# Optimization experiments

Measured on AMD Instinct MI355X. Metric: run time of the kernel, lower is better.

Reference implementation:

```python
import jax, jax.numpy as jnp
import numpy as np

NHEAD, DK, DV = 8, 32, 32
GRAPH = [[1,2,3,6,7],[1,2,4],[1,3,5],[2,4],[3,5],[1,6,8,12],[1,7,9,13],[6,8,10],[7,9,13],[8,10],[9,11],[9,12,14],[11,13,15],[12,14,16],[13,15,17],[14,16],[15,17]]
_idx = np.zeros((17,5), np.int32); _val = np.zeros((17,5), bool)
for _i, _nb in enumerate(GRAPH):
    for _j, _n in enumerate(_nb):
        _idx[_i,_j] = _n-1; _val[_i,_j] = True
NBR_IDX = jnp.asarray(_idx)            # (17,5) neighbor table (pad idx 0)
NBR_VALID = jnp.asarray(_val)          # (17,5) valid-neighbor mask
ATT_MASK = jnp.asarray(np.concatenate([_val, np.ones((17,2), bool)], 1))  # (17,7): 5 local + 2 global keys
INV_SQRT_DK = float(1.0/np.sqrt(DK))

def _ln_c(x, g, b, eps=1e-6):
    # LayerNorm over channel axis of (B,C,L)
    m = x.mean(1, keepdims=True)
    v = x.var(1, keepdims=True)
    return (x - m) * jax.lax.rsqrt(v + eps) * g[None,:,None] + b[None,:,None]

def _bn3(x, g, b, eps=1e-5):
    # BatchNorm1d (training batch stats) per channel over (B,L); x:(B,C,L)
    m = x.mean((0,2), keepdims=True)
    v = x.var((0,2), keepdims=True)
    return (x - m) * jax.lax.rsqrt(v + eps) * g[None,:,None] + b[None,:,None]

def _pos_ffn(x, w1, b1, w2, b2, g, b):
    # x:(B,C,L); Linear over C, relu, Linear back, residual, BatchNorm1d
    h = jax.nn.relu(jnp.einsum('bcl,hc->bhl', x, w1) + b1[None,:,None])
    y = jnp.einsum('bhl,ch->bcl', h, w2) + b2[None,:,None] + x
    return _bn3(y, g, b)

def _unfold(t):
    # t:(B,C,17) -> (B,C,5,17): per-node 5-wide neighbor window, zero padded
    g = t[:,:,NBR_IDX]                              # (B,C,17,5)
    g = jnp.where(NBR_VALID[None,None], g, 0.0)
    return jnp.transpose(g, (0,1,3,2))

def _sju(xn, ax, wq,bq,wk,bk,wv,bv, bng,bnb, f1w,f1b,f2w,f2b,fg,fb):
    B, C, L = xn.shape
    q = (jnp.einsum('oc,bcl->bol', wq, xn) + bq[None,:,None]).reshape(B,NHEAD,DK,L)
    kx = jnp.einsum('oc,bcl->bol', wk, xn) + bk[None,:,None]
    vx = jnp.einsum('oc,bcl->bol', wv, xn) + bv[None,:,None]
    k = _unfold(kx).reshape(B,NHEAD,DK,5,L)
    v = _unfold(vx).reshape(B,NHEAD,DV,5,L)
    ak = (jnp.einsum('oc,bcal->boal', wk, ax) + bk[None,:,None,None]).reshape(B,NHEAD,DK,2,L)
    av = (jnp.einsum('oc,bcal->boal', wv, ax) + bv[None,:,None,None]).reshape(B,NHEAD,DV,2,L)
    k = jnp.concatenate([k, ak], 3)                 # (B,H,dk,7,L)
    v = jnp.concatenate([v, av], 3)
    pre = jnp.einsum('bhdl,bhdwl->bhwl', q, k) * INV_SQRT_DK
    pre = jnp.where(ATT_MASK.T[None,None], pre, -jnp.inf)
    a = jax.nn.softmax(pre, axis=2)
    att = jnp.einsum('bhwl,bhdwl->bhdl', a, v).reshape(B,C,L)
    ret = _bn3(xn + att, bng, bnb)
    return _pos_ffn(ret, f1w,f1b,f2w,f2b,fg,fb)

def _sru(x, y, wq,bq,wk,bk,wv,bv, bng,bnb, f1w,f1b,f2w,f2b,fg,fb):
    # x:(B,C) relay, y:(B,C,Ly) keys/values
    B, C = x.shape
    q = (x @ wq.T + bq).reshape(B,NHEAD,DK)
    k = (jnp.einsum('oc,bcl->bol', wk, y) + bk[None,:,None]).reshape(B,NHEAD,DK,-1)
    v = (jnp.einsum('oc,bcl->bol', wv, y) + bv[None,:,None]).reshape(B,NHEAD,DV,-1)
    a = jax.nn.softmax(jnp.einsum('bhd,bhdl->bhl', q, k) * INV_SQRT_DK, axis=2)
    att = jnp.einsum('bhl,bhdl->bhd', a, v).reshape(B,C)
    ret = _bn3((x + att)[:,:,None], bng, bnb)
    return _pos_ffn(ret, f1w,f1b,f2w,f2b,fg,fb)[:,:,0]

def _forward(data, ln_g, ln_b, jq_w, jq_b, jk_w, jk_b, jv_w, jv_b, jbn_g, jbn_b, jf1_w, jf1_b, jf2_w, jf2_b, jfbn_g, jfbn_b, rq_w, rq_b, rk_w, rk_b, rv_w, rv_b, rbn_g, rbn_b, rf1_w, rf1_b, rf2_w, rf2_b, rfbn_g, rfbn_b):
    B, C, V, T = data.shape
    embs = jnp.transpose(data, (0,3,1,2)).reshape(B*T, C, V)   # fold time into batch
    nodes = embs
    relay = embs.mean(2)                                       # (BT,C)
    # ax: per node the 2 extra keys = its own original embedding + relay (fixed across layers)
    ax = jnp.stack([embs, jnp.broadcast_to(relay[:,:,None], embs.shape)], axis=2)  # (BT,C,2,V)
    for i in range(ln_g.shape[0]):
        xn = _ln_c(nodes, ln_g[i], ln_b[i])
        nodes = jax.nn.leaky_relu(_sju(xn, ax, jq_w[i],jq_b[i],jk_w[i],jk_b[i],jv_w[i],jv_b[i],jbn_g[i],jbn_b[i],jf1_w[i],jf1_b[i],jf2_w[i],jf2_b[i],jfbn_g[i],jfbn_b[i]), 0.01)
        y = jnp.concatenate([relay[:,:,None], nodes], axis=2)   # (BT,C,18)
        relay = jax.nn.leaky_relu(_sru(relay, y, rq_w[i],rq_b[i],rk_w[i],rk_b[i],rv_w[i],rv_b[i],rbn_g[i],rbn_b[i],rf1_w[i],rf1_b[i],rf2_w[i],rf2_b[i],rfbn_g[i],rfbn_b[i]), 0.01)
    return jnp.transpose(nodes.reshape(B,T,C,V), (0,2,3,1))

def setup_inputs():
    key = jax.random.key(0)
    Lyr, C, DIN, B, T, V = 2, 256, 1024, 4, 256, 17
    ks = jax.random.split(key, 40)
    ctr = [0]
    def nxt():
        k = ks[ctr[0]]; ctr[0] += 1; return k
    def w(shape, s=0.05):
        return jax.random.normal(nxt(), shape, jnp.float32) * s
    ones = lambda: jnp.ones((Lyr, C), jnp.float32)
    zeros = lambda: jnp.zeros((Lyr, C), jnp.float32)
    inp = {'data': jax.random.normal(nxt(), (B,C,V,T), jnp.float32),
           'ln_g': ones(), 'ln_b': zeros()}
    for p in ('j', 'r'):
        inp[p+'q_w'] = w((Lyr,C,C)); inp[p+'q_b'] = w((Lyr,C))
        inp[p+'k_w'] = w((Lyr,C,C)); inp[p+'k_b'] = w((Lyr,C))
        inp[p+'v_w'] = w((Lyr,C,C)); inp[p+'v_b'] = w((Lyr,C))
        inp[p+'bn_g'] = ones(); inp[p+'bn_b'] = zeros()
        inp[p+'f1_w'] = w((Lyr,DIN,C)); inp[p+'f1_b'] = w((Lyr,DIN))
        inp[p+'f2_w'] = w((Lyr,C,DIN)); inp[p+'f2_b'] = w((Lyr,C))
        inp[p+'fbn_g'] = ones(); inp[p+'fbn_b'] = zeros()
    return inp

def reference(data, ln_g, ln_b, jq_w, jq_b, jk_w, jk_b, jv_w, jv_b, jbn_g, jbn_b, jf1_w, jf1_b, jf2_w, jf2_b, jfbn_g, jfbn_b, rq_w, rq_b, rk_w, rk_b, rv_w, rv_b, rbn_g, rbn_b, rf1_w, rf1_b, rf2_w, rf2_b, rfbn_g, rfbn_b):
    return _forward(data, ln_g, ln_b, jq_w, jq_b, jk_w, jk_b, jv_w, jv_b, jbn_g, jbn_b, jf1_w, jf1_b, jf2_w, jf2_b, jfbn_g, jfbn_b, rq_w, rq_b, rk_w, rk_b, rv_w, rv_b, rbn_g, rbn_b, rf1_w, rf1_b, rf2_w, rf2_b, rfbn_g, rfbn_b)
```

## Files before the change

kernel.cpp:

```cpp
#include <hip/hip_runtime.h>
#include <hip/hip_bf16.h>


using bf16 = __hip_bfloat16;
typedef __attribute__((ext_vector_type(8))) short bf16x8v;
typedef __attribute__((ext_vector_type(4))) float f32x4;

namespace {
constexpr int kBT = 1024;
constexpr int kC = 256;
constexpr int kV = 17;
constexpr int kT = 256;
constexpr int kDIN = 1024;
constexpr int kRows = kBT * kV;
constexpr int kRowsE = kRows + kBT;
constexpr float kInvSqrtDk = 0.17677669529663687f;
constexpr size_t SZ_BIG = (size_t)kRows * kC;
}

__constant__ int c_nbi[17][5] = {
    {0, 1, 2, 5, 6},   {0, 1, 3, 0, 0},   {0, 2, 4, 0, 0},  {1, 3, 0, 0, 0},
    {2, 4, 0, 0, 0},   {0, 5, 7, 11, 0},  {0, 6, 8, 12, 0}, {5, 7, 9, 0, 0},
    {6, 8, 12, 0, 0},  {7, 9, 0, 0, 0},   {8, 10, 0, 0, 0}, {8, 11, 13, 0, 0},
    {10, 12, 14, 0, 0},{11, 13, 15, 0, 0},{12, 14, 16, 0, 0},
    {13, 15, 0, 0, 0}, {14, 16, 0, 0, 0}};
__constant__ int c_ncnt[17] = {5, 3, 3, 2, 2, 4, 4, 3, 3, 2, 2, 3, 3, 3, 3, 2, 2};

__device__ inline float bf2f(unsigned short s) {
  unsigned int u = ((unsigned int)s) << 16;
  float f;
  __builtin_memcpy(&f, &u, 4);
  return f;
}
__device__ inline unsigned short f2bf(float f) {
  unsigned int u;
  __builtin_memcpy(&u, &f, 4);
  unsigned int r = (u + 0x7fffu + ((u >> 16) & 1u)) >> 16;
  return (unsigned short)r;
}
__device__ inline float4 ldbf4(const bf16* p) {
  ushort4 u = *(const ushort4*)p;
  return make_float4(bf2f(u.x), bf2f(u.y), bf2f(u.z), bf2f(u.w));
}
__device__ inline void stbf4(bf16* p, float4 v) {
  ushort4 u = make_ushort4(f2bf(v.x), f2bf(v.y), f2bf(v.z), f2bf(v.w));
  *(ushort4*)p = u;
}
__device__ inline float dot4(float4 a, float4 b) {
  return a.x * b.x + a.y * b.y + a.z * b.z + a.w * b.w;
}

__device__ inline void async16(const bf16* g, bf16* l) {
  __builtin_amdgcn_global_load_lds(
      (const __attribute__((address_space(1))) void*)g,
      (__attribute__((address_space(3))) void*)l, 16, 0, 0);
}

template <int KT>
__global__ __launch_bounds__(256) void k_mfma_gemm(
    const bf16* __restrict__ A, const bf16* __restrict__ W,
    const float* __restrict__ bias, const float* __restrict__ res,
    float* __restrict__ outF, bf16* __restrict__ outB,
    const float* __restrict__ bnScI, const float* __restrict__ bnShI,
    float* __restrict__ partOut, int nbPart, int N, int flags) {
  __shared__ bf16 As[2][128 * 64];
  __shared__ bf16 Bs[2][128 * 64];
  const int tid = threadIdx.x;
  const int wave = tid >> 6;
  const int lane = tid & 63;
  const int row0 = blockIdx.x * 128;
  const int col0 = blockIdx.y * 128;

  const int sub = lane >> 2;
  const int kq = (lane & 3) * 8;
  const int rg0 = (2 * wave + 0) * 16;
  const int rg1 = (2 * wave + 1) * 16;
  const bf16* ag0 = A + (size_t)(row0 + rg0 + sub) * KT + kq;
  const bf16* ag1 = A + (size_t)(row0 + rg1 + sub) * KT + kq;
  const bf16* bg0 = W + (size_t)(col0 + rg0 + sub) * KT + kq;
  const bf16* bg1 = W + (size_t)(col0 + rg1 + sub) * KT + kq;

  const int wm = wave >> 1, wn = wave & 1;
  const int fr = lane & 15;
  const int fk = (lane >> 4) * 8;

  f32x4 acc[4][4];
#pragma unroll
  for (int i = 0; i < 4; ++i)
#pragma unroll
    for (int j = 0; j < 4; ++j) acc[i][j] = (f32x4){0.f, 0.f, 0.f, 0.f};

#define STAGE64(buf, koff)                                   \
  do {                                                       \
    _Pragma("unroll") for (int kc = 0; kc < 2; ++kc) {       \
      const int off = (koff) + kc * 32;                      \
      async16(ag0 + off, &As[(buf)][kc * 4096 + rg0 * 32]);  \
      async16(ag1 + off, &As[(buf)][kc * 4096 + rg1 * 32]);  \
      async16(bg0 + off, &Bs[(buf)][kc * 4096 + rg0 * 32]);  \
      async16(bg1 + off, &Bs[(buf)][kc * 4096 + rg1 * 32]);  \
    }                                                        \
  } while (0)

  STAGE64(0, 0);
  __syncthreads();

  for (int k0 = 0; k0 < KT; k0 += 64) {
    const int cur = (k0 >> 6) & 1;
    if (k0 + 64 < KT) STAGE64(cur ^ 1, k0 + 64);
#pragma unroll
    for (int kc = 0; kc < 2; ++kc) {
      bf16x8v af[4], bfv[4];
#pragma unroll
      for (int i = 0; i < 4; ++i)
        af[i] = *(const bf16x8v*)&As[cur][kc * 4096 +
                                          (wm * 64 + i * 16 + fr) * 32 + fk];
#pragma unroll
      for (int j = 0; j < 4; ++j)
        bfv[j] = *(const bf16x8v*)&Bs[cur][kc * 4096 +
                                           (wn * 64 + j * 16 + fr) * 32 + fk];
#pragma unroll
      for (int i = 0; i < 4; ++i)
#pragma unroll
        for (int j = 0; j < 4; ++j)
          acc[i][j] = __builtin_amdgcn_mfma_f32_16x16x32_bf16(af[i], bfv[j],
                                                              acc[i][j], 0, 0,
                                                              0);
    }
    __syncthreads();
  }
#undef STAGE64

  if (flags & 4) {
    unsigned short* cs = (unsigned short*)As;
#pragma unroll
    for (int j = 0; j < 4; ++j) {
      int lc = wn * 64 + j * 16 + fr;
      float bv = bias ? bias[col0 + lc] : 0.f;
#pragma unroll
      for (int i = 0; i < 4; ++i) {
        int lr = wm * 64 + i * 16 + (lane >> 4) * 4;
#pragma unroll
        for (int r = 0; r < 4; ++r) {
          float v = acc[i][j][r] + bv;
          if (flags & 1) v = fmaxf(v, 0.f);
          cs[(lr + r) * 128 + lc] = f2bf(v);
        }
      }
    }
    __syncthreads();
#pragma unroll
    for (int p = 0; p < 8; ++p) {
      int lr = p * 16 + (tid >> 4);
      int lc = (tid & 15) * 8;
      *(bf16x8v*)&outB[(size_t)(row0 + lr) * N + col0 + lc] =
          *(const bf16x8v*)&cs[lr * 128 + lc];
    }
  } else {
    const int crow = row0 + wm * 64;
    const int ccol = col0 + wn * 64;
    float colS[4] = {0.f, 0.f, 0.f, 0.f};
    float colQ[4] = {0.f, 0.f, 0.f, 0.f};
#pragma unroll
    for (int j = 0; j < 4; ++j) {
      int col = ccol + j * 16 + fr;
      float bv = bias ? bias[col] : 0.f;
      float rsc = 1.f, rsh = 0.f;
      if (flags & 8) { rsc = bnScI[col]; rsh = bnShI[col]; }
#pragma unroll
      for (int i = 0; i < 4; ++i) {
        int rowb = crow + i * 16 + (lane >> 4) * 4;
#pragma unroll
        for (int r = 0; r < 4; ++r) {
          size_t row = (size_t)(rowb + r);
          float v = acc[i][j][r] + bv;
          if (res) v += res[row * N + col] * rsc + rsh;
          if (flags & 1) v = fmaxf(v, 0.f);
          outF[row * N + col] = v;
          colS[j] += v;
          colQ[j] += v * v;
        }
      }
    }
    if (flags & 8) {
#pragma unroll
      for (int j = 0; j < 4; ++j) {
        colS[j] += __shfl_xor(colS[j], 16);
        colS[j] += __shfl_xor(colS[j], 32);
        colQ[j] += __shfl_xor(colQ[j], 16);
        colQ[j] += __shfl_xor(colQ[j], 32);
      }
      float* sred = (float*)As;
      float* qred = sred + 4 * 64;
      if (lane < 16) {
#pragma unroll
        for (int j = 0; j < 4; ++j) {
          sred[wave * 64 + j * 16 + fr] = colS[j];
          qred[wave * 64 + j * 16 + fr] = colQ[j];
        }
      }
      __syncthreads();
      if (tid < 128) {
        int wn2 = tid >> 6, c = tid & 63;
        float s = sred[wn2 * 64 + c] + sred[(wn2 | 2) * 64 + c];
        float q = qred[wn2 * 64 + c] + qred[(wn2 | 2) * 64 + c];
        int col = col0 + wn2 * 64 + c;
        partOut[(size_t)blockIdx.x * kC + col] = s;
        partOut[(size_t)(nbPart + blockIdx.x) * kC + col] = q;
      }
    }
  }
}

__global__ __launch_bounds__(256) void k_xform_in(const float* __restrict__ data,
                                                  float* __restrict__ nodes,
                                                  bf16* __restrict__ embs_bf) {
  __shared__ float tile[32][33];
  int ct = blockIdx.x * 32, tt = blockIdx.y * 32;
  int bv = blockIdx.z;
  int b = bv / kV, v = bv - b * kV;
  int tx = threadIdx.x & 31, ty = threadIdx.x >> 5;
  for (int i = ty; i < 32; i += 8)
    tile[i][tx] = data[(((size_t)b * kC + ct + i) * kV + v) * kT + tt + tx];
  __syncthreads();
  for (int i = ty; i < 32; i += 8) {
    size_t s = (size_t)b * kT + tt + i;
    size_t idx = (s * kV + v) * kC + ct + tx;
    float val = tile[tx][i];
    nodes[idx] = val;
    embs_bf[idx] = __float2bfloat16(val);
  }
}

__global__ __launch_bounds__(256) void k_xform_out(const float* __restrict__ Z,
                                                   const float* __restrict__ scale,
                                                   const float* __restrict__ shift,
                                                   float* __restrict__ out) {
  __shared__ float tile[32][33];
  int ct = blockIdx.x * 32, tt = blockIdx.y * 32;
  int bv = blockIdx.z;
  int b = bv / kV, v = bv - b * kV;
  int tx = threadIdx.x & 31, ty = threadIdx.x >> 5;
  float sc = scale[ct + tx], sh = shift[ct + tx];
  for (int i = ty; i < 32; i += 8) {
    size_t s = (size_t)b * kT + tt + i;
    float val = Z[(s * kV + v) * kC + ct + tx] * sc + sh;
    val = (val > 0.f) ? val : 0.01f * val;
    tile[i][tx] = val;
  }
  __syncthreads();
  for (int i = ty; i < 32; i += 8)
    out[(((size_t)b * kC + ct + i) * kV + v) * kT + tt + tx] = tile[tx][i];
}

__global__ __launch_bounds__(256) void k_relay_init(const float* __restrict__ nodes,
                                                    bf16* __restrict__ relay0_bf) {
  int t = threadIdx.x;
  int s = blockIdx.x * 4 + (t >> 6);
  int c4 = (t & 63) * 4;
  float4 acc = make_float4(0.f, 0.f, 0.f, 0.f);
#pragma unroll
  for (int v = 0; v < kV; ++v) {
    float4 x = *(const float4*)(nodes + ((size_t)s * kV + v) * kC + c4);
    acc.x += x.x; acc.y += x.y; acc.z += x.z; acc.w += x.w;
  }
  float4 r = make_float4(acc.x / 17.f, acc.y / 17.f, acc.z / 17.f, acc.w / 17.f);
  stbf4(relay0_bf + (size_t)s * kC + c4, r);
}

__global__ __launch_bounds__(256) void k_layernorm(const float* __restrict__ X,
                                                   const float* __restrict__ g,
                                                   const float* __restrict__ b,
                                                   float* __restrict__ O,
                                                   bf16* __restrict__ Ob) {
  int t = threadIdx.x;
  int row = blockIdx.x * 4 + (t >> 6);
  int c4 = (t & 63) * 4;
  size_t i = (size_t)row * kC + c4;
  float4 x = *(const float4*)(X + i);
  float s = x.x + x.y + x.z + x.w;
  float q = dot4(x, x);
#pragma unroll
  for (int o = 32; o >= 1; o >>= 1) {
    s += __shfl_xor(s, o);
    q += __shfl_xor(q, o);
  }
  float m = s * (1.f / 256.f);
  float var = q * (1.f / 256.f) - m * m;
  float rs = rsqrtf(var + 1e-6f);
  float4 g4 = *(const float4*)(g + c4);
  float4 b4 = *(const float4*)(b + c4);
  float4 o4 = make_float4((x.x - m) * rs * g4.x + b4.x,
                          (x.y - m) * rs * g4.y + b4.y,
                          (x.z - m) * rs * g4.z + b4.z,
                          (x.w - m) * rs * g4.w + b4.w);
  *(float4*)(O + i) = o4;
  stbf4(Ob + i, o4);
}

__global__ __launch_bounds__(256) void k_attn_sat(const bf16* __restrict__ qkv,
                                                  const bf16* __restrict__ akav,
                                                  float* __restrict__ z,
                                                  float* __restrict__ part,
                                                  int nb) {
  __shared__ float sS[4][256];
  __shared__ float qS[4][256];
  int t = threadIdx.x;
  int w = t >> 6;
  int rl = blockIdx.x * 4 + w;
  int lane = t & 63;
  int s = rl / kV, l = rl - s * kV;
  int c4 = lane * 4;
  float4 q = ldbf4(qkv + (size_t)rl * 768 + c4);
  int cnt = c_ncnt[l];
  float sc[7];
  int nrow[5];
#pragma unroll
  for (int wd = 0; wd < 5; ++wd) {
    nrow[wd] = s * kV + c_nbi[l][wd];
    float4 k = ldbf4(qkv + (size_t)nrow[wd] * 768 + 256 + c4);
    float p = dot4(q, k);
    p += __shfl_xor(p, 1, 8);
    p += __shfl_xor(p, 2, 8);
    p += __shfl_xor(p, 4, 8);
    sc[wd] = (wd < cnt) ? p * kInvSqrtDk : -1e30f;
  }
  {
    float4 k = ldbf4(akav + (size_t)rl * 1024 + c4);
    float p = dot4(q, k);
    p += __shfl_xor(p, 1, 8);
    p += __shfl_xor(p, 2, 8);
    p += __shfl_xor(p, 4, 8);
    sc[5] = p * kInvSqrtDk;
  }
  {
    float4 k = ldbf4(akav + (size_t)(kRows + s) * 1024 + c4);
    float p = dot4(q, k);
    p += __shfl_xor(p, 1, 8);
    p += __shfl_xor(p, 2, 8);
    p += __shfl_xor(p, 4, 8);
    sc[6] = p * kInvSqrtDk;
  }
  float mx = sc[0];
#pragma unroll
  for (int wd = 1; wd < 7; ++wd) mx = fmaxf(mx, sc[wd]);
  float den = 0.f;
#pragma unroll
  for (int wd = 0; wd < 7; ++wd) {
    sc[wd] = __expf(sc[wd] - mx);
    den += sc[wd];
  }
  float inv = 1.f / den;
  float4 acc = make_float4(0.f, 0.f, 0.f, 0.f);
#pragma unroll
  for (int wd = 0; wd < 5; ++wd) {
    float4 v = ldbf4(qkv + (size_t)nrow[wd] * 768 + 512 + c4);
    acc.x += sc[wd] * v.x; acc.y += sc[wd] * v.y;
    acc.z += sc[wd] * v.z; acc.w += sc[wd] * v.w;
  }
  {
    float4 v = ldbf4(akav + (size_t)rl * 1024 + 256 + c4);
    acc.x += sc[5] * v.x; acc.y += sc[5] * v.y;
    acc.z += sc[5] * v.z; acc.w += sc[5] * v.w;
  }
  {
    float4 v = ldbf4(akav + (size_t)(kRows + s) * 1024 + 256 + c4);
    acc.x += sc[6] * v.x; acc.y += sc[6] * v.y;
    acc.z += sc[6] * v.z; acc.w += sc[6] * v.w;
  }
  size_t zi = (size_t)rl * kC + c4;
  float4 xv = *(const float4*)(z + zi);
  float4 o = make_float4(xv.x + acc.x * inv, xv.y + acc.y * inv,
                         xv.z + acc.z * inv, xv.w + acc.w * inv);
  *(float4*)(z + zi) = o;
  sS[w][c4 + 0] = o.x; sS[w][c4 + 1] = o.y;
  sS[w][c4 + 2] = o.z; sS[w][c4 + 3] = o.w;
  qS[w][c4 + 0] = o.x * o.x; qS[w][c4 + 1] = o.y * o.y;
  qS[w][c4 + 2] = o.z * o.z; qS[w][c4 + 3] = o.w * o.w;
  __syncthreads();
  float ps = sS[0][t] + sS[1][t] + sS[2][t] + sS[3][t];
  float pq = qS[0][t] + qS[1][t] + qS[2][t] + qS[3][t];
  part[(size_t)blockIdx.x * kC + t] = ps;
  part[(size_t)(nb + blockIdx.x) * kC + t] = pq;
}

__global__ __launch_bounds__(256) void k_bn_finalize(const float* __restrict__ part,
                                                     int nb, float inv_n,
                                                     const float* __restrict__ g,
                                                     const float* __restrict__ b,
                                                     float* __restrict__ scale,
                                                     float* __restrict__ shift) {
  int c = blockIdx.x;
  int t = threadIdx.x;
  float s = 0.f, q = 0.f;
  for (int i = t; i < nb; i += 256) {
    s += part[(size_t)i * kC + c];
    q += part[(size_t)(nb + i) * kC + c];
  }
#pragma unroll
  for (int o = 32; o >= 1; o >>= 1) {
    s += __shfl_xor(s, o);
    q += __shfl_xor(q, o);
  }
  __shared__ float ws[4], wq[4];
  int wid = t >> 6;
  if ((t & 63) == 0) { ws[wid] = s; wq[wid] = q; }
  __syncthreads();
  if (t == 0) {
    float S = ws[0] + ws[1] + ws[2] + ws[3];
    float Q = wq[0] + wq[1] + wq[2] + wq[3];
    float m = S * inv_n;
    float var = Q * inv_n - m * m;
    float sc = g[c] * rsqrtf(var + 1e-5f);
    scale[c] = sc;
    shift[c] = b[c] - m * sc;
  }
}

__global__ __launch_bounds__(256) void k_bn_apply(const float* __restrict__ Z,
                                                  const float* __restrict__ scale,
                                                  const float* __restrict__ shift,
                                                  float* __restrict__ outF,
                                                  bf16* __restrict__ outB,
                                                  int leaky) {
  int t = threadIdx.x;
  int row = blockIdx.x * 4 + (t >> 6);
  int c4 = (t & 63) * 4;
  size_t i = (size_t)row * kC + c4;
  float4 z = *(const float4*)(Z + i);
  float4 sc = *(const float4*)(scale + c4);
  float4 sh = *(const float4*)(shift + c4);
  float4 v = make_float4(z.x * sc.x + sh.x, z.y * sc.y + sh.y,
                         z.z * sc.z + sh.z, z.w * sc.w + sh.w);
  if (leaky) {
    v.x = (v.x > 0.f) ? v.x : 0.01f * v.x;
    v.y = (v.y > 0.f) ? v.y : 0.01f * v.y;
    v.z = (v.z > 0.f) ? v.z : 0.01f * v.z;
    v.w = (v.w > 0.f) ? v.w : 0.01f * v.w;
  }
  if (outF) *(float4*)(outF + i) = v;
  if (outB) stbf4(outB + i, v);
}

__global__ __launch_bounds__(256) void k_bn_ln(
    const float* __restrict__ Z, const float* __restrict__ scale,
    const float* __restrict__ shift, const float* __restrict__ g,
    const float* __restrict__ b, float* __restrict__ xnOut,
    bf16* __restrict__ actOut) {
  int t = threadIdx.x;
  int row = blockIdx.x * 4 + (t >> 6);
  int c4 = (t & 63) * 4;
  size_t i = (size_t)row * kC + c4;
  float4 z = *(const float4*)(Z + i);
  float4 sc = *(const float4*)(scale + c4);
  float4 sh = *(const float4*)(shift + c4);
  float4 v = make_float4(z.x * sc.x + sh.x, z.y * sc.y + sh.y,
                         z.z * sc.z + sh.z, z.w * sc.w + sh.w);
  v.x = (v.x > 0.f) ? v.x : 0.01f * v.x;
  v.y = (v.y > 0.f) ? v.y : 0.01f * v.y;
  v.z = (v.z > 0.f) ? v.z : 0.01f * v.z;
  v.w = (v.w > 0.f) ? v.w : 0.01f * v.w;
  float s = v.x + v.y + v.z + v.w;
  float q = dot4(v, v);
#pragma unroll
  for (int o = 32; o >= 1; o >>= 1) {
    s += __shfl_xor(s, o);
    q += __shfl_xor(q, o);
  }
  float m = s * (1.f / 256.f);
  float var = q * (1.f / 256.f) - m * m;
  float rs = rsqrtf(var + 1e-6f);
  float4 g4 = *(const float4*)(g + c4);
  float4 b4 = *(const float4*)(b + c4);
  float4 o4 = make_float4((v.x - m) * rs * g4.x + b4.x,
                          (v.y - m) * rs * g4.y + b4.y,
                          (v.z - m) * rs * g4.z + b4.z,
                          (v.w - m) * rs * g4.w + b4.w);
  *(float4*)(xnOut + i) = o4;
  stbf4(actOut + i, o4);
}

struct CvtTab {
  const float* src[12];
  bf16* dst[12];
  int n[12];
};
__global__ __launch_bounds__(256) void k_cvt_multi(CvtTab t) {
  int c = blockIdx.y;
  int i = (blockIdx.x * 256 + threadIdx.x) * 4;
  if (i >= t.n[c]) return;
  float4 v = *(const float4*)(t.src[c] + i);
  stbf4(t.dst[c] + i, v);
}

struct BiasTab {
  const float* src[10];
  float* dst[10];
};
__global__ __launch_bounds__(256) void k_bias_cat(BiasTab t) {
  t.dst[blockIdx.x][threadIdx.x] = t.src[blockIdx.x][threadIdx.x];
}

extern "C" void kernel_launch(void* const* d_in, const int* in_sizes, int n_in,
                              void* d_out, int out_size, void* d_ws, size_t ws_size,
                              hipStream_t stream) {
  const float* data = (const float*)d_in[0];
  const float* ln_g = (const float*)d_in[1];
  const float* ln_b = (const float*)d_in[2];
  const float* jq_w = (const float*)d_in[3];
  const float* jq_b = (const float*)d_in[4];
  const float* jk_w = (const float*)d_in[5];
  const float* jk_b = (const float*)d_in[6];
  const float* jv_w = (const float*)d_in[7];
  const float* jv_b = (const float*)d_in[8];
  const float* jbn_g = (const float*)d_in[9];
  const float* jbn_b = (const float*)d_in[10];
  const float* jf1_w = (const float*)d_in[11];
  const float* jf1_b = (const float*)d_in[12];
  const float* jf2_w = (const float*)d_in[13];
  const float* jf2_b = (const float*)d_in[14];
  const float* jfbn_g = (const float*)d_in[15];
  const float* jfbn_b = (const float*)d_in[16];
  float* out = (float*)d_out;

  float* f = (float*)d_ws;
  float* nodes = f;    f += SZ_BIG;
  float* xn = f;       f += SZ_BIG;
  float* part = f;     f += 2 * (kRows / 4) * kC;
  float* scale = f;    f += kC;
  float* shift = f;    f += kC;
  float* cb_jqkv = f;  f += 2 * 768;
  float* cb_kv4 = f;   f += 1024;

  bf16* bfa = (bf16*)f;
  bf16* act_bf = bfa;   bfa += SZ_BIG;
  bf16* embsX_bf = bfa; bfa += (size_t)kRowsE * kC;
  bf16* P = bfa;        bfa += (size_t)kRows * kDIN;
  bf16* akavBuf = bfa;  bfa += (size_t)kRowsE * 1024;
  bf16* Wjqkv = bfa;    bfa += 2 * 768 * 256;
  bf16* Wkv4 = bfa;     bfa += 1024 * 256;
  bf16* Wjf1 = bfa;     bfa += 2 * 1024 * 256;
  bf16* Wjf2 = bfa;     bfa += 2 * 256 * 1024;

  bf16* relay0_bf = embsX_bf + SZ_BIG;
  bf16* qkv_bf = P;
  bf16* h_bf = P;
  float* y2 = xn;

  auto gemm = [&](const bf16* A, const bf16* W, const float* bias,
                  const float* res, float* oF, bf16* oB, const float* bnScI,
                  const float* bnShI, float* partOut, int nbPart, int M, int N,
                  int K, int flags) {
    dim3 g(M / 128, N / 128);
    if (K == 256)
      k_mfma_gemm<256><<<g, 256, 0, stream>>>(A, W, bias, res, oF, oB, bnScI,
                                              bnShI, partOut, nbPart, N, flags);
    else
      k_mfma_gemm<1024><<<g, 256, 0, stream>>>(A, W, bias, res, oF, oB, bnScI,
                                               bnShI, partOut, nbPart, N,
                                               flags);
  };

  {
    CvtTab t;
    for (int i = 0; i < 2; ++i) {
      const size_t om = (size_t)i * kC * kC;
      const float* s3[3] = {jq_w + om, jk_w + om, jv_w + om};
      bf16* d3[3] = {Wjqkv + (size_t)i * 768 * 256,
                     Wjqkv + (size_t)i * 768 * 256 + 65536,
                     Wjqkv + (size_t)i * 768 * 256 + 131072};
      for (int j = 0; j < 3; ++j) {
        t.src[i * 3 + j] = s3[j];
        t.dst[i * 3 + j] = d3[j];
        t.n[i * 3 + j] = 65536;
      }
    }
    t.src[6] = jk_w;                 t.dst[6] = Wkv4;               t.n[6] = 65536;
    t.src[7] = jv_w;                 t.dst[7] = Wkv4 + 65536;       t.n[7] = 65536;
    t.src[8] = jk_w + (size_t)65536; t.dst[8] = Wkv4 + 131072;      t.n[8] = 65536;
    t.src[9] = jv_w + (size_t)65536; t.dst[9] = Wkv4 + 196608;      t.n[9] = 65536;
    t.src[10] = jf1_w; t.dst[10] = Wjf1; t.n[10] = 2 * 1024 * 256;
    t.src[11] = jf2_w; t.dst[11] = Wjf2; t.n[11] = 2 * 256 * 1024;
    k_cvt_multi<<<dim3(512, 12), 256, 0, stream>>>(t);
  }
  {
    BiasTab t;
    for (int i = 0; i < 2; ++i) {
      t.src[i * 3 + 0] = jq_b + (size_t)i * kC;
      t.src[i * 3 + 1] = jk_b + (size_t)i * kC;
      t.src[i * 3 + 2] = jv_b + (size_t)i * kC;
      t.dst[i * 3 + 0] = cb_jqkv + i * 768;
      t.dst[i * 3 + 1] = cb_jqkv + i * 768 + 256;
      t.dst[i * 3 + 2] = cb_jqkv + i * 768 + 512;
    }
    t.src[6] = jk_b;       t.dst[6] = cb_kv4;
    t.src[7] = jv_b;       t.dst[7] = cb_kv4 + 256;
    t.src[8] = jk_b + kC;  t.dst[8] = cb_kv4 + 512;
    t.src[9] = jv_b + kC;  t.dst[9] = cb_kv4 + 768;
    k_bias_cat<<<10, 256, 0, stream>>>(t);
  }

  k_xform_in<<<dim3(8, 8, 4 * kV), 256, 0, stream>>>(data, nodes, embsX_bf);
  k_relay_init<<<kBT / 4, 256, 0, stream>>>(nodes, relay0_bf);

  gemm(embsX_bf, Wkv4, cb_kv4, nullptr, nullptr, akavBuf, nullptr, nullptr,
       nullptr, 0, kRowsE, 1024, 256, 4);

  k_layernorm<<<kRows / 4, 256, 0, stream>>>(nodes, ln_g, ln_b, xn, act_bf);

  for (int i = 0; i < 2; ++i) {
    const size_t ob = (size_t)i * kC, ofb1 = (size_t)i * kDIN;
    const bf16* Wj = Wjqkv + (size_t)i * 768 * 256;
    const bf16* Wf1 = Wjf1 + (size_t)i * 1024 * 256;
    const bf16* Wf2 = Wjf2 + (size_t)i * 256 * 1024;
    const float* cbj = cb_jqkv + i * 768;
    const int nbA = kRows / 4;
    const int nbG = kRows / 128;

    gemm(act_bf, Wj, cbj, nullptr, nullptr, qkv_bf, nullptr, nullptr, nullptr,
         0, kRows, 768, 256, 4);
    k_attn_sat<<<kRows / 4, 256, 0, stream>>>(qkv_bf, akavBuf + (size_t)i * 512,
                                              xn, part, nbA);
    k_bn_finalize<<<kC, 256, 0, stream>>>(part, nbA, 1.f / kRows, jbn_g + ob,
                                          jbn_b + ob, scale, shift);
    k_bn_apply<<<kRows / 4, 256, 0, stream>>>(xn, scale, shift, nullptr,
                                              act_bf, 0);
    gemm(act_bf, Wf1, jf1_b + ofb1, nullptr, nullptr, h_bf, nullptr, nullptr,
         nullptr, 0, kRows, 1024, 256, 4 | 1);
    gemm(h_bf, Wf2, jf2_b + ob, xn, y2, nullptr, scale, shift, part, nbG,
         kRows, 256, 1024, 2 | 8);
    k_bn_finalize<<<kC, 256, 0, stream>>>(part, nbG, 1.f / kRows, jfbn_g + ob,
                                          jfbn_b + ob, scale, shift);
    if (i == 0) {
      k_bn_ln<<<kRows / 4, 256, 0, stream>>>(y2, scale, shift, ln_g + kC,
                                             ln_b + kC, xn, act_bf);
    }
  }

  k_xform_out<<<dim3(8, 8, 4 * kV), 256, 0, stream>>>(y2, scale, shift, out);
  (void)in_sizes; (void)n_in; (void)out_size; (void)ws_size;
}
```

Measured before the change: 431.7 us.

## Halve GEMM K-step to 32 and cut LDS to raise occupancy

The MFMA GEMM stages 32-wide K slices instead of 64-wide ones, which halves shared memory from 64KB to 32KB per block, and adds a launch-bounds hint of 4 blocks per CU. The goal is to fit more resident blocks per CU so more loads are in flight and latency is better hidden. In exchange it doubles the number of loop iterations and barriers per K, and the occupancy hint may limit registers, which could cause spills given the 64 accumulator floats per lane. The epilogue's shared-memory reuse now points at the smaller raw buffer.

Result: no change. 431.8 us (+0.0%).

```diff
diff --git a/kernel.cpp b/kernel.cpp
--- a/kernel.cpp
+++ b/kernel.cpp
@@ -57,14 +57,15 @@
 }
 
 template <int KT>
-__global__ __launch_bounds__(256) void k_mfma_gemm(
+__global__ __launch_bounds__(256, 4) void k_mfma_gemm(
     const bf16* __restrict__ A, const bf16* __restrict__ W,
     const float* __restrict__ bias, const float* __restrict__ res,
     float* __restrict__ outF, bf16* __restrict__ outB,
     const float* __restrict__ bnScI, const float* __restrict__ bnShI,
     float* __restrict__ partOut, int nbPart, int N, int flags) {
-  __shared__ bf16 As[2][128 * 64];
-  __shared__ bf16 Bs[2][128 * 64];
+  __shared__ __align__(16) char smem_raw[32768];
+  bf16* As = (bf16*)smem_raw;
+  bf16* Bs = (bf16*)(smem_raw + 16384);
   const int tid = threadIdx.x;
   const int wave = tid >> 6;
   const int lane = tid & 63;
@@ -90,48 +91,42 @@
 #pragma unroll
     for (int j = 0; j < 4; ++j) acc[i][j] = (f32x4){0.f, 0.f, 0.f, 0.f};
 
-#define STAGE64(buf, koff)                                   \
-  do {                                                       \
-    _Pragma("unroll") for (int kc = 0; kc < 2; ++kc) {       \
-      const int off = (koff) + kc * 32;                      \
-      async16(ag0 + off, &As[(buf)][kc * 4096 + rg0 * 32]);  \
-      async16(ag1 + off, &As[(buf)][kc * 4096 + rg1 * 32]);  \
-      async16(bg0 + off, &Bs[(buf)][kc * 4096 + rg0 * 32]);  \
-      async16(bg1 + off, &Bs[(buf)][kc * 4096 + rg1 * 32]);  \
-    }                                                        \
+#define STAGE32(buf, koff)                              \
+  do {                                                  \
+    async16(ag0 + (koff), As + (buf) * 4096 + rg0 * 32); \
+    async16(ag1 + (koff), As + (buf) * 4096 + rg1 * 32); \
+    async16(bg0 + (koff), Bs + (buf) * 4096 + rg0 * 32); \
+    async16(bg1 + (koff), Bs + (buf) * 4096 + rg1 * 32); \
   } while (0)
 
-  STAGE64(0, 0);
+  STAGE32(0, 0);
   __syncthreads();
 
-  for (int k0 = 0; k0 < KT; k0 += 64) {
-    const int cur = (k0 >> 6) & 1;
-    if (k0 + 64 < KT) STAGE64(cur ^ 1, k0 + 64);
-#pragma unroll
-    for (int kc = 0; kc < 2; ++kc) {
-      bf16x8v af[4], bfv[4];
-#pragma unroll
-      for (int i = 0; i < 4; ++i)
-        af[i] = *(const bf16x8v*)&As[cur][kc * 4096 +
-                                          (wm * 64 + i * 16 + fr) * 32 + fk];
+  for (int k0 = 0; k0 < KT; k0 += 32) {
+    const int cur = (k0 >> 5) & 1;
+    if (k0 + 32 < KT) STAGE32(cur ^ 1, k0 + 32);
+    bf16x8v af[4], bfv[4];
+#pragma unroll
+    for (int i = 0; i < 4; ++i)
+      af[i] = *(const bf16x8v*)&As[cur * 4096 +
+                                   (wm * 64 + i * 16 + fr) * 32 + fk];
+#pragma unroll
+    for (int j = 0; j < 4; ++j)
+      bfv[j] = *(const bf16x8v*)&Bs[cur * 4096 +
+                                    (wn * 64 + j * 16 + fr) * 32 + fk];
+#pragma unroll
+    for (int i = 0; i < 4; ++i)
 #pragma unroll
       for (int j = 0; j < 4; ++j)
-        bfv[j] = *(const bf16x8v*)&Bs[cur][kc * 4096 +
-                                           (wn * 64 + j * 16 + fr) * 32 + fk];
-#pragma unroll
-      for (int i = 0; i < 4; ++i)
-#pragma unroll
-        for (int j = 0; j < 4; ++j)
-          acc[i][j] = __builtin_amdgcn_mfma_f32_16x16x32_bf16(af[i], bfv[j],
-                                                              acc[i][j], 0, 0,
-                                                              0);
-    }
+        acc[i][j] = __builtin_amdgcn_mfma_f32_16x16x32_bf16(af[i], bfv[j],
+                                                            acc[i][j], 0, 0,
+                                                            0);
     __syncthreads();
   }
-#undef STAGE64
+#undef STAGE32
 
   if (flags & 4) {
-    unsigned short* cs = (unsigned short*)As;
+    unsigned short* cs = (unsigned short*)smem_raw;
 #pragma unroll
     for (int j = 0; j < 4; ++j) {
       int lc = wn * 64 + j * 16 + fr;
@@ -189,7 +184,7 @@
         colQ[j] += __shfl_xor(colQ[j], 16);
         colQ[j] += __shfl_xor(colQ[j], 32);
       }
-      float* sred = (float*)As;
+      float* sred = (float*)smem_raw;
       float* qred = sred + 4 * 64;
       if (lane < 16) {
 #pragma unroll
```

## Remap GEMM workgroups per XCD and use fine-grained vmcnt waits in K loop

Applied to the files above, without the earlier changes.

Block indices are remapped so that consecutive logical tiles land on the same XCD, which is meant to improve L2 reuse of A and W tiles across the MI355X's chiplets. The K loop now waits with explicit s_waitcnt vmcnt counts and raw s_barrier instead of __syncthreads. This lets the next stage's async LDS loads stay in flight while the current stage is computed, and the loop is unrolled. Partial-stat outputs are indexed by the remapped row tile, and an added barrier protects LDS reuse in the reduction. The hand-written waitcnt counts assume exactly 8 outstanding loads per stage, which is fragile if the compiler emits other memory operations.

Result: no change. 439.4 us (+1.8%).

```diff
diff --git a/kernel.cpp b/kernel.cpp
--- a/kernel.cpp
+++ b/kernel.cpp
@@ -68,8 +68,20 @@
   const int tid = threadIdx.x;
   const int wave = tid >> 6;
   const int lane = tid & 63;
-  const int row0 = blockIdx.x * 128;
-  const int col0 = blockIdx.y * 128;
+
+  const int gx = gridDim.x;
+  const int nColT = gridDim.y;
+  const int nwg = gx * nColT;
+  const int flat = blockIdx.y * gx + blockIdx.x;
+  const int q = nwg >> 3, rmd = nwg & 7;
+  const int xcd = flat & 7;
+  const int wgid =
+      (xcd < rmd ? xcd * (q + 1) : rmd * (q + 1) + (xcd - rmd) * q) +
+      (flat >> 3);
+  const int rowT = wgid / nColT;
+  const int colT = wgid - rowT * nColT;
+  const int row0 = rowT * 128;
+  const int col0 = colT * 128;
 
   const int sub = lane >> 2;
   const int kq = (lane & 3) * 8;
@@ -102,11 +114,17 @@
   } while (0)
 
   STAGE64(0, 0);
-  __syncthreads();
-
+
+#pragma unroll
   for (int k0 = 0; k0 < KT; k0 += 64) {
     const int cur = (k0 >> 6) & 1;
-    if (k0 + 64 < KT) STAGE64(cur ^ 1, k0 + 64);
+    if (k0 + 64 < KT) {
+      STAGE64(cur ^ 1, k0 + 64);
+      asm volatile("s_waitcnt vmcnt(8)" ::: "memory");
+    } else {
+      asm volatile("s_waitcnt vmcnt(0)" ::: "memory");
+    }
+    asm volatile("s_barrier" ::: "memory");
 #pragma unroll
     for (int kc = 0; kc < 2; ++kc) {
       bf16x8v af[4], bfv[4];
@@ -126,7 +144,7 @@
                                                               acc[i][j], 0, 0,
                                                               0);
     }
-    __syncthreads();
+    asm volatile("s_barrier" ::: "memory");
   }
 #undef STAGE64
 
@@ -191,6 +209,7 @@
       }
       float* sred = (float*)As;
       float* qred = sred + 4 * 64;
+      __syncthreads();
       if (lane < 16) {
 #pragma unroll
         for (int j = 0; j < 4; ++j) {
@@ -202,10 +221,10 @@
       if (tid < 128) {
         int wn2 = tid >> 6, c = tid & 63;
         float s = sred[wn2 * 64 + c] + sred[(wn2 | 2) * 64 + c];
-        float q = qred[wn2 * 64 + c] + qred[(wn2 | 2) * 64 + c];
+        float q2 = qred[wn2 * 64 + c] + qred[(wn2 | 2) * 64 + c];
         int col = col0 + wn2 * 64 + c;
-        partOut[(size_t)blockIdx.x * kC + col] = s;
-        partOut[(size_t)(nbPart + blockIdx.x) * kC + col] = q;
+        partOut[(size_t)rowT * kC + col] = s;
+        partOut[(size_t)(nbPart + rowT) * kC + col] = q2;
       }
     }
   }
```
